# Optimization experiments

Measured on AMD Instinct MI355X. Metric: run time of the kernel, lower is better.

The kernel has to match this reference:

```python
import jax, jax.numpy as jnp
import numpy as np

NEG_INF = -1e9

def apply_rope(x, positions, head_dim, theta):
    # x: [B, S, H, Dh]; positions: [S] int32
    half = head_dim // 2
    fraction = (2.0 / head_dim) * jnp.arange(half, dtype=jnp.float32)  # [Dh/2]
    timescale = theta ** fraction
    angle = positions.astype(jnp.float32)[:, None] / timescale  # [S, Dh/2]
    sin = jnp.sin(angle)[None, :, None, :]  # [1,S,1,Dh/2]
    cos = jnp.cos(angle)[None, :, None, :]
    x1, x2 = jnp.split(x, 2, axis=-1)
    out = jnp.concatenate([x1 * cos - x2 * sin, x2 * cos + x1 * sin], axis=-1)
    return out.astype(x.dtype)

def setup_inputs() -> dict:
    key = jax.random.key(0)
    B, S, D = 2, 2048, 2048
    Q, N, H = 16, 4, 128
    ks = jax.random.split(key, 5)
    scale = 1.0 / np.sqrt(D)
    return {
        "x": jax.random.normal(ks[0], (B, S, D), dtype=jnp.float32),
        "positions": jnp.arange(S, dtype=jnp.int32),
        "Wq": jax.random.normal(ks[1], (Q, D, H), dtype=jnp.float32) * scale,
        "Wk": jax.random.normal(ks[2], (N, D, H), dtype=jnp.float32) * scale,
        "Wv": jax.random.normal(ks[3], (N, D, H), dtype=jnp.float32) * scale,
        "Wo": jax.random.normal(ks[4], (Q, H, D), dtype=jnp.float32) * scale,
    }

def reference(x, positions, Wq, Wk, Wv, Wo):
    head_dim = Wq.shape[-1]
    theta = 10000.0
    head_repeats = Wq.shape[0] // Wk.shape[0]  # GQA repeat factor

    q_BSQH = jnp.einsum('BSD,QDH->BSQH', x, Wq)
    q_BSQH = apply_rope(q_BSQH, positions, head_dim, theta)
    k_BTNH = jnp.einsum('BSD,NDH->BSNH', x, Wk)
    k_BTNH = apply_rope(k_BTNH, positions, head_dim, theta)
    v_BTNH = jnp.einsum('BSD,NDH->BSNH', x, Wv)

    k_BTQH = jnp.repeat(k_BTNH, head_repeats, axis=2)
    v_BTQH = jnp.repeat(v_BTNH, head_repeats, axis=2)

    scores_BQST = jnp.einsum('BSQH,BTQH->BQST', q_BSQH, k_BTQH) / jnp.sqrt(
        jnp.asarray(head_dim, dtype=x.dtype))
    S = q_BSQH.shape[1]
    causal = jnp.tril(jnp.ones((1, 1, S, S), dtype=jnp.bool_))
    scores_BQST = jnp.where(causal, scores_BQST, NEG_INF)
    weights_BQST = jax.nn.softmax(scores_BQST, axis=-1)
    out_BSQH = jnp.einsum('BQST,BTQH->BSQH', weights_BQST, v_BTQH)
    o_BSD = jnp.einsum('BSQH,QHD->BSD', out_BSQH, Wo)
    return o_BSD
```

## Files before the change

### kernel.cpp

```cpp
#include <hip/hip_runtime.h>
#include <math.h>

#define BB 2
#define SS 2048
#define DD 2048
#define QH 16
#define NKV 4
#define HD 128
#define REP 4
#define NEG_INF_F (-1e9f)

typedef __bf16 bfrag __attribute__((ext_vector_type(8)));
typedef float  ffrag __attribute__((ext_vector_type(4)));

__device__ inline unsigned short f2bf(float f) {
    unsigned u = __builtin_bit_cast(unsigned, f);
    u += 0x7fff + ((u >> 16) & 1);
    return (unsigned short)(u >> 16);
}
__device__ inline float bf2f(unsigned short u) {
    unsigned v = (unsigned)u << 16;
    return __builtin_bit_cast(float, v);
}
__device__ inline bfrag ld_frag(const unsigned short* p) {
    uint4 u = *(const uint4*)p;
    return __builtin_bit_cast(bfrag, u);
}
__device__ inline void async16(const void* g, void* l) {
    __builtin_amdgcn_global_load_lds(
        (const __attribute__((address_space(1))) unsigned int*)g,
        (__attribute__((address_space(3))) unsigned int*)l, 16, 0, 0);
}
__device__ inline unsigned pkbf(float a, float b) {
    unsigned short ua = __builtin_bit_cast(unsigned short, (__bf16)a);
    unsigned short ub = __builtin_bit_cast(unsigned short, (__bf16)b);
    return (unsigned)ua | ((unsigned)ub << 16);
}

__global__ __launch_bounds__(256) void prep_kernel(
    const float* __restrict__ x, unsigned short* __restrict__ xb,
    const float* __restrict__ Wq, const float* __restrict__ Wk,
    const float* __restrict__ Wv, const float* __restrict__ Wo,
    unsigned short* __restrict__ Wqkvt, unsigned short* __restrict__ Wot)
{
    __shared__ float tile[32][33];
    const int blk = blockIdx.x;
    const int tid = threadIdx.x;

    if (blk < 4096) {
        const int i = blk * 2048 + tid * 8;
        float4 a = *(const float4*)(x + i);
        float4 b = *(const float4*)(x + i + 4);
        unsigned short o[8];
        o[0] = f2bf(a.x); o[1] = f2bf(a.y); o[2] = f2bf(a.z); o[3] = f2bf(a.w);
        o[4] = f2bf(b.x); o[5] = f2bf(b.y); o[6] = f2bf(b.z); o[7] = f2bf(b.w);
        *(uint4*)(xb + i) = *(uint4*)o;
        return;
    }

    const float* in;
    unsigned short* out;
    int R, C, bx, by;
    if (blk < 10240) {
        const int lw = blk - 4096;
        const int z  = lw >> 8;
        const int r  = lw & 255;
        bx = r & 3; by = r >> 2;
        R = 2048; C = 128;
        if (z < 16)      { in = Wq + (size_t)z * 2048 * 128;
                           out = Wqkvt + (size_t)z * 128 * 2048; }
        else if (z < 20) { in = Wk + (size_t)(z - 16) * 2048 * 128;
                           out = Wqkvt + (size_t)(16 + (z - 16)) * 128 * 2048; }
        else             { in = Wv + (size_t)(z - 20) * 2048 * 128;
                           out = Wqkvt + (size_t)(20 + (z - 20)) * 128 * 2048; }
    } else {
        const int lw = blk - 10240;
        bx = lw & 63; by = lw >> 6;
        R = 2048; C = 2048;
        in = Wo; out = Wot;
    }
    const int c0 = bx * 32, r0 = by * 32;
    const int tx = tid & 31, ty = tid >> 5;
    #pragma unroll
    for (int k = 0; k < 4; ++k)
        tile[ty + 8 * k][tx] = in[(size_t)(r0 + ty + 8 * k) * C + c0 + tx];
    __syncthreads();
    #pragma unroll
    for (int k = 0; k < 4; ++k)
        out[(size_t)(c0 + ty + 8 * k) * R + r0 + tx] =
            f2bf(tile[tx][ty + 8 * k]);
}

__global__ __launch_bounds__(256) void gemm_bt_kernel(
    const unsigned short* __restrict__ A,
    const unsigned short* __restrict__ Bt,
    unsigned short* __restrict__ q_out, unsigned short* __restrict__ k_out,
    unsigned short* __restrict__ vt_out, float* __restrict__ f_out,
    int mode)
{
    const int m0 = blockIdx.x * 128;
    const int n0 = blockIdx.y * 128;
    const int tid  = threadIdx.x;
    const int w    = tid >> 6, lane = tid & 63;
    const int l16  = lane & 15, quad = lane >> 4;
    const int wm = (w >> 1) * 64, wn = (w & 1) * 64;
    const int sw8 = l16 & 7;

    __shared__ unsigned short As[2][128 * 64];
    __shared__ unsigned short Bs[2][128 * 64];

    ffrag acc[4][4];
    #pragma unroll
    for (int mi = 0; mi < 4; ++mi)
        #pragma unroll
        for (int ni = 0; ni < 4; ++ni)
            acc[mi][ni] = (ffrag){0.f, 0.f, 0.f, 0.f};

    auto stage = [&](int d, int k0) {
        #pragma unroll
        for (int j = 0; j < 4; ++j) {
            const int i   = j * 256 + tid;
            const int row = i >> 3;
            const int sl  = (i & 7) ^ (row & 7);
            async16(&A [(size_t)(m0 + row) * 2048 + k0 + sl * 8],
                    (char*)&As[d][0] + i * 16);
            async16(&Bt[(size_t)(n0 + row) * 2048 + k0 + sl * 8],
                    (char*)&Bs[d][0] + i * 16);
        }
    };

    stage(0, 0);
    __syncthreads();
    int cur = 0;
    for (int k0 = 0; k0 < 2048; k0 += 64) {
        if (k0 + 64 < 2048) stage(cur ^ 1, k0 + 64);

        #pragma unroll
        for (int c2 = 0; c2 < 2; ++c2) {
            bfrag af[4], bfr[4];
            #pragma unroll
            for (int mi = 0; mi < 4; ++mi)
                af[mi] = ld_frag(&As[cur][(wm + mi * 16 + l16) * 64
                                          + (((c2 * 4 + quad) ^ sw8) * 8)]);
            #pragma unroll
            for (int ni = 0; ni < 4; ++ni)
                bfr[ni] = ld_frag(&Bs[cur][(wn + ni * 16 + l16) * 64
                                           + (((c2 * 4 + quad) ^ sw8) * 8)]);
            #pragma unroll
            for (int mi = 0; mi < 4; ++mi)
                #pragma unroll
                for (int ni = 0; ni < 4; ++ni)
                    acc[mi][ni] = __builtin_amdgcn_mfma_f32_16x16x32_bf16(
                        af[mi], bfr[ni], acc[mi][ni], 0, 0, 0);
        }

        __syncthreads();
        cur ^= 1;
    }

    if (mode == 0) {
        #pragma unroll
        for (int mi = 0; mi < 4; ++mi)
            #pragma unroll
            for (int ni = 0; ni < 4; ++ni) {
                const int col = n0 + wn + ni * 16 + l16;
                #pragma unroll
                for (int r = 0; r < 4; ++r) {
                    const int row = m0 + wm + mi * 16 + quad * 4 + r;
                    f_out[(size_t)row * 2048 + col] = acc[mi][ni][r];
                }
            }
    } else if (n0 < 2560) {
        unsigned short* dst;
        int colbase, stride;
        if (n0 < 2048)      { dst = q_out; colbase = n0;        stride = 2048; }
        else                { dst = k_out; colbase = n0 - 2048; stride = 512;  }
        #pragma unroll
        for (int mi = 0; mi < 4; ++mi)
            #pragma unroll
            for (int ni = 0; ni < 4; ++ni) {
                const int col = colbase + wn + ni * 16 + l16;
                #pragma unroll
                for (int r = 0; r < 4; ++r) {
                    const int row = m0 + wm + mi * 16 + quad * 4 + r;
                    dst[(size_t)row * stride + col] = f2bf(acc[mi][ni][r]);
                }
            }
    } else {
        const int c3 = n0 - 2560;
        #pragma unroll
        for (int mi = 0; mi < 4; ++mi)
            #pragma unroll
            for (int ni = 0; ni < 4; ++ni) {
                const int col = c3 + wn + ni * 16 + l16;
                const int nh = col >> 7, h = col & 127;
                const int row0 = m0 + wm + mi * 16 + quad * 4;
                const int b = row0 >> 11, s = row0 & 2047;
                unsigned short pk[4];
                #pragma unroll
                for (int r = 0; r < 4; ++r) pk[r] = f2bf(acc[mi][ni][r]);
                *(uint2*)&vt_out[(((size_t)b * NKV + nh) * HD + h) * SS + s] =
                    *(uint2*)pk;
            }
    }
}

__global__ void rope_kernel(unsigned short* __restrict__ q,
                            unsigned short* __restrict__ k,
                            const int* __restrict__ positions)
{
    const int qpairs = BB * SS * QH * 64;
    const int kpairs = BB * SS * NKV * 64;
    int idx = blockIdx.x * blockDim.x + threadIdx.x;
    unsigned short* base;
    int nh;
    if (idx < qpairs) { base = q; nh = QH; }
    else {
        idx -= qpairs;
        if (idx >= kpairs) return;
        base = k; nh = NKV;
    }
    const int hh   = idx & 63;
    const int rest = idx >> 6;
    const int head = rest % nh;
    const int bs   = rest / nh;
    const int s    = bs % SS;

    unsigned short* p = base + ((size_t)bs * nh + head) * HD;
    const float pos = (float)positions[s];
    const float inv_ts = powf(10000.0f, -(float)hh * (1.0f / 64.0f));
    const float angle = pos * inv_ts;
    const float sn = sinf(angle), cs = cosf(angle);
    const float sc_ = (nh == QH) ? 0.08838834764831845f : 1.0f;
    const float x1 = bf2f(p[hh]), x2 = bf2f(p[hh + 64]);
    p[hh]      = f2bf((x1 * cs - x2 * sn) * sc_);
    p[hh + 64] = f2bf((x2 * cs + x1 * sn) * sc_);
}

__global__ __launch_bounds__(256, 2) void attn_kernel(
    const unsigned short* __restrict__ qb,
    const unsigned short* __restrict__ kb,
    const unsigned short* __restrict__ vt,
    unsigned short* __restrict__ o)
{
    int f = blockIdx.y * 16 + blockIdx.x;
    f = (f & 7) * 64 + (f >> 3);
    const int bh = f >> 4;
    const int bx = f & 15;

    const int b  = bh / QH, qh = bh % QH;
    const int n  = qh / REP;

    const int tid  = threadIdx.x;
    const int w    = tid >> 6;
    const int lane = tid & 63;
    const int l16  = lane & 15;
    const int quad = lane >> 4;
    const int sw   = l16 & 7;

    __shared__ unsigned short Ks[2][2][64][64];
    __shared__ unsigned short Vs[2][128][64];
    __shared__ unsigned short Ps[4][16][72];

    const unsigned short* kbase = kb + (size_t)b * (SS * NKV * HD) + n * HD;
    const unsigned short* vbase = vt + ((size_t)b * NKV + n) * HD * SS;

    for (int ph = 0; ph < 2; ++ph) {
        const int tile = ph == 0 ? (31 - bx) : bx;
        const int s0 = tile * 64;
        const int rbase = s0 + w * 16 + quad * 4;
        const int thr   = w * 16 + l16;

        bfrag qf[4];
        {
            const unsigned short* qp =
                qb + ((size_t)(b * SS + s0 + w * 16 + l16) * QH + qh) * HD
                   + quad * 8;
            #pragma unroll
            for (int c = 0; c < 4; ++c) qf[c] = ld_frag(qp + c * 32);
        }
        ffrag oacc[8];
        #pragma unroll
        for (int t = 0; t < 8; ++t) oacc[t] = (ffrag){0.f, 0.f, 0.f, 0.f};
        float mr = -1e30f, lr = 0.0f;

        #pragma unroll
        for (int j = 0; j < 4; ++j) {
            const int s = j * 256 + tid;
            {   const int cc = s >> 9, t = (s >> 3) & 63;
                const int sl = (s & 7) ^ (t & 7);
                async16(kbase + (size_t)t * (NKV * HD) + cc * 64 + sl * 8,
                        (char*)&Ks[0][0][0][0] + s * 16);
            }
            {   const int h = s >> 3, sl = (s & 7) ^ (h & 7);
                async16(vbase + (size_t)h * SS + sl * 8,
                        (char*)&Vs[0][0][0] + s * 16);
            }
        }
        __syncthreads();

        int p = 0;
        for (int t0 = 0; t0 <= s0; t0 += 64, p ^= 1) {
            if (t0 + 64 <= s0) {
                const int tn = t0 + 64;
                #pragma unroll
                for (int j = 0; j < 4; ++j) {
                    const int s = j * 256 + tid;
                    {   const int cc = s >> 9, t = (s >> 3) & 63;
                        const int sl = (s & 7) ^ (t & 7);
                        async16(kbase + (size_t)(tn + t) * (NKV * HD)
                                      + cc * 64 + sl * 8,
                                (char*)&Ks[p ^ 1][0][0][0] + s * 16);
                    }
                    {   const int h = s >> 3, sl = (s & 7) ^ (h & 7);
                        async16(vbase + (size_t)h * SS + tn + sl * 8,
                                (char*)&Vs[p ^ 1][0][0] + s * 16);
                    }
                }
            }

            ffrag sc[4];
            #pragma unroll
            for (int t = 0; t < 4; ++t) sc[t] = (ffrag){0.f, 0.f, 0.f, 0.f};
            __builtin_amdgcn_s_setprio(1);
            #pragma unroll
            for (int c = 0; c < 4; ++c) {
                const int cc = c >> 1, cb = (c & 1) * 4;
                #pragma unroll
                for (int t = 0; t < 4; ++t) {
                    bfrag kfr = ld_frag(
                        &Ks[p][cc][t * 16 + l16][((cb + quad) ^ sw) * 8]);
                    sc[t] = __builtin_amdgcn_mfma_f32_16x16x32_bf16(
                        kfr, qf[c], sc[t], 0, 0, 0);
                }
            }
            __builtin_amdgcn_s_setprio(0);

            const bool diag = (t0 == s0);
            if (diag) {
                #pragma unroll
                for (int t = 0; t < 4; ++t) {
                    const int col0 = t * 16 + quad * 4;
                    #pragma unroll
                    for (int r = 0; r < 4; ++r)
                        if (col0 + r > thr) sc[t][r] = NEG_INF_F;
                }
            }

            float tmax;
            {
                float a0 = fmaxf(fmaxf(sc[0][0], sc[0][1]),
                                 fmaxf(sc[0][2], sc[0][3]));
                float a1 = fmaxf(fmaxf(sc[1][0], sc[1][1]),
                                 fmaxf(sc[1][2], sc[1][3]));
                float a2 = fmaxf(fmaxf(sc[2][0], sc[2][1]),
                                 fmaxf(sc[2][2], sc[2][3]));
                float a3 = fmaxf(fmaxf(sc[3][0], sc[3][1]),
                                 fmaxf(sc[3][2], sc[3][3]));
                tmax = fmaxf(fmaxf(a0, a1), fmaxf(a2, a3));
            }
            tmax = fmaxf(tmax, __shfl_xor(tmax, 16));
            tmax = fmaxf(tmax, __shfl_xor(tmax, 32));

            if (__any(tmax > mr + 8.0f)) {
                const float mnew  = fmaxf(mr, tmax);
                const float alpha = __expf(mr - mnew);
                lr *= alpha;
                mr = mnew;
                #pragma unroll
                for (int r = 0; r < 4; ++r) {
                    const float ar =
                        __shfl(alpha, (lane & 48) | (quad * 4 + r));
                    #pragma unroll
                    for (int t = 0; t < 8; ++t) oacc[t][r] *= ar;
                }
            }

            float ps = 0.f;
            #pragma unroll
            for (int t = 0; t < 4; ++t) {
                const float p0 = __expf(sc[t][0] - mr);
                const float p1 = __expf(sc[t][1] - mr);
                const float p2 = __expf(sc[t][2] - mr);
                const float p3 = __expf(sc[t][3] - mr);
                ps += (p0 + p1) + (p2 + p3);
                uint2 pk2;
                pk2.x = pkbf(p0, p1);
                pk2.y = pkbf(p2, p3);
                *(uint2*)&Ps[w][l16][t * 16 + quad * 4] = pk2;
            }
            ps += __shfl_xor(ps, 16);
            ps += __shfl_xor(ps, 32);
            lr += ps;

            __builtin_amdgcn_s_setprio(1);
            #pragma unroll
            for (int c = 0; c < 2; ++c) {
                bfrag pf = ld_frag(&Ps[w][l16][c * 32 + quad * 8]);
                #pragma unroll
                for (int t = 0; t < 8; ++t) {
                    bfrag vf = ld_frag(
                        &Vs[p][t * 16 + l16][((c * 4 + quad) ^ sw) * 8]);
                    oacc[t] = __builtin_amdgcn_mfma_f32_16x16x32_bf16(
                        pf, vf, oacc[t], 0, 0, 0);
                }
            }
            __builtin_amdgcn_s_setprio(0);

            __syncthreads();
        }

        #pragma unroll
        for (int r = 0; r < 4; ++r) {
            const float lrr  = __shfl(lr, (lane & 48) | (quad * 4 + r));
            const float invl = 1.0f / lrr;
            const int row = rbase + r;
            unsigned short* op = o + ((size_t)(b * SS + row) * QH + qh) * HD;
            #pragma unroll
            for (int t = 0; t < 8; ++t)
                op[t * 16 + l16] = f2bf(oacc[t][r] * invl);
        }
    }
}

extern "C" void kernel_launch(void* const* d_in, const int* in_sizes, int n_in,
                              void* d_out, int out_size, void* d_ws,
                              size_t ws_size, hipStream_t stream)
{
    const float* x         = (const float*)d_in[0];
    const int*   positions = (const int*)d_in[1];
    const float* Wq        = (const float*)d_in[2];
    const float* Wk        = (const float*)d_in[3];
    const float* Wv        = (const float*)d_in[4];
    const float* Wo        = (const float*)d_in[5];
    float* out = (float*)d_out;

    char* ws = (char*)d_ws;
    unsigned short* xb    = (unsigned short*)ws;
    unsigned short* Wqkvt = (unsigned short*)(ws + (16u << 20));
    unsigned short* Wot   = (unsigned short*)(ws + (28u << 20));
    unsigned short* qbf   = (unsigned short*)(ws + (36u << 20));
    unsigned short* kbf   = (unsigned short*)(ws + (52u << 20));
    unsigned short* vtb   = (unsigned short*)(ws + (56u << 20));
    unsigned short* opre  = xb;

    prep_kernel<<<14336, 256, 0, stream>>>(x, xb, Wq, Wk, Wv, Wo, Wqkvt, Wot);

    gemm_bt_kernel<<<dim3(32, 24), 256, 0, stream>>>(
        xb, Wqkvt, qbf, kbf, vtb, nullptr, 1);

    const int pairs = BB * SS * (QH + NKV) * 64;
    rope_kernel<<<(pairs + 255) / 256, 256, 0, stream>>>(qbf, kbf, positions);

    dim3 g2(16, BB * QH);
    attn_kernel<<<g2, 256, 0, stream>>>(qbf, kbf, vtb, opre);

    gemm_bt_kernel<<<dim3(32, 16), 256, 0, stream>>>(
        opre, Wot, nullptr, nullptr, nullptr, out, 0);
}
```

Before: 312.5 us.

## Shrink K tile to 32 keys, decouple K/V buffering, raise occupancy to three blocks

Splits the key loop into 32-key steps with K double-buffered per 32 keys while V stays at 64-key granularity, loading the next V tile every other step. Waves whose query rows lie entirely above a diagonal 32-key tile skip the score, softmax and PV work for it, which cuts wasted causal-masked compute. Shared-memory buffers shrink and launch bounds rise to 3 blocks per CU for more occupancy. The cost is twice as many barriers per key range and smaller MFMA batches per step, with register pressure capped by the tighter launch bound.

```diff
diff --git a/kernel.cpp b/kernel.cpp
--- a/kernel.cpp
+++ b/kernel.cpp
@@ -237,7 +237,7 @@
     p[hh + 64] = f2bf((x2 * cs + x1 * sn) * sc_);
 }
 
-__global__ __launch_bounds__(256, 2) void attn_kernel(
+__global__ __launch_bounds__(256, 3) void attn_kernel(
     const unsigned short* __restrict__ qb,
     const unsigned short* __restrict__ kb,
     const unsigned short* __restrict__ vt,
@@ -258,9 +258,9 @@
     const int quad = lane >> 4;
     const int sw   = l16 & 7;
 
-    __shared__ unsigned short Ks[2][2][64][64];
+    __shared__ unsigned short Ks[2][2][32][64];
     __shared__ unsigned short Vs[2][128][64];
-    __shared__ unsigned short Ps[4][16][72];
+    __shared__ unsigned short Ps[4][16][36];
 
     const unsigned short* kbase = kb + (size_t)b * (SS * NKV * HD) + n * HD;
     const unsigned short* vbase = vt + ((size_t)b * NKV + n) * HD * SS;
@@ -285,127 +285,130 @@
         float mr = -1e30f, lr = 0.0f;
 
         #pragma unroll
+        for (int j = 0; j < 2; ++j) {
+            const int i = j * 256 + tid;
+            const int cc = i >> 8, t = (i >> 3) & 31, sl = i & 7;
+            async16(kbase + (size_t)t * (NKV * HD) + cc * 64
+                          + ((sl ^ (t & 7)) * 8),
+                    (char*)&Ks[0][0][0][0] + i * 16);
+        }
+        #pragma unroll
         for (int j = 0; j < 4; ++j) {
-            const int s = j * 256 + tid;
-            {   const int cc = s >> 9, t = (s >> 3) & 63;
-                const int sl = (s & 7) ^ (t & 7);
-                async16(kbase + (size_t)t * (NKV * HD) + cc * 64 + sl * 8,
-                        (char*)&Ks[0][0][0][0] + s * 16);
-            }
-            {   const int h = s >> 3, sl = (s & 7) ^ (h & 7);
-                async16(vbase + (size_t)h * SS + sl * 8,
-                        (char*)&Vs[0][0][0] + s * 16);
-            }
+            const int i = j * 256 + tid;
+            const int h = i >> 3, sl = i & 7;
+            async16(vbase + (size_t)h * SS + ((sl ^ (h & 7)) * 8),
+                    (char*)&Vs[0][0][0] + i * 16);
         }
         __syncthreads();
 
-        int p = 0;
-        for (int t0 = 0; t0 <= s0; t0 += 64, p ^= 1) {
-            if (t0 + 64 <= s0) {
-                const int tn = t0 + 64;
+        for (int t0 = 0; t0 <= s0 + 32; t0 += 32) {
+            const int pk = (t0 >> 5) & 1;
+            const int pv = (t0 >> 6) & 1;
+
+            if (t0 <= s0) {
+                #pragma unroll
+                for (int j = 0; j < 2; ++j) {
+                    const int i = j * 256 + tid;
+                    const int cc = i >> 8, t = (i >> 3) & 31, sl = i & 7;
+                    async16(kbase + (size_t)(t0 + 32 + t) * (NKV * HD)
+                                  + cc * 64 + ((sl ^ (t & 7)) * 8),
+                            (char*)&Ks[pk ^ 1][0][0][0] + i * 16);
+                }
+            }
+            if ((t0 & 32) == 0 && t0 + 64 <= s0 + 32) {
                 #pragma unroll
                 for (int j = 0; j < 4; ++j) {
-                    const int s = j * 256 + tid;
-                    {   const int cc = s >> 9, t = (s >> 3) & 63;
-                        const int sl = (s & 7) ^ (t & 7);
-                        async16(kbase + (size_t)(tn + t) * (NKV * HD)
-                                      + cc * 64 + sl * 8,
-                                (char*)&Ks[p ^ 1][0][0][0] + s * 16);
+                    const int i = j * 256 + tid;
+                    const int h = i >> 3, sl = i & 7;
+                    async16(vbase + (size_t)h * SS + t0 + 64
+                                  + ((sl ^ (h & 7)) * 8),
+                            (char*)&Vs[pv ^ 1][0][0] + i * 16);
+                }
+            }
+
+            const int toff = t0 - s0;
+            if (toff <= w * 16 + 15) {
+                ffrag sc[2];
+                sc[0] = (ffrag){0.f, 0.f, 0.f, 0.f};
+                sc[1] = (ffrag){0.f, 0.f, 0.f, 0.f};
+                __builtin_amdgcn_s_setprio(1);
+                #pragma unroll
+                for (int c = 0; c < 4; ++c) {
+                    const int cc = c >> 1, cb = (c & 1) * 4;
+                    #pragma unroll
+                    for (int ts = 0; ts < 2; ++ts) {
+                        bfrag kfr = ld_frag(
+                            &Ks[pk][cc][ts * 16 + l16][((cb + quad) ^ sw) * 8]);
+                        sc[ts] = __builtin_amdgcn_mfma_f32_16x16x32_bf16(
+                            kfr, qf[c], sc[ts], 0, 0, 0);
                     }
-                    {   const int h = s >> 3, sl = (s & 7) ^ (h & 7);
-                        async16(vbase + (size_t)h * SS + tn + sl * 8,
-                                (char*)&Vs[p ^ 1][0][0] + s * 16);
+                }
+                __builtin_amdgcn_s_setprio(0);
+
+                if (toff >= 0) {
+                    #pragma unroll
+                    for (int ts = 0; ts < 2; ++ts) {
+                        const int col0 = toff + ts * 16 + quad * 4;
+                        #pragma unroll
+                        for (int r = 0; r < 4; ++r)
+                            if (col0 + r > thr) sc[ts][r] = NEG_INF_F;
                     }
                 }
-            }
-
-            ffrag sc[4];
-            #pragma unroll
-            for (int t = 0; t < 4; ++t) sc[t] = (ffrag){0.f, 0.f, 0.f, 0.f};
-            __builtin_amdgcn_s_setprio(1);
-            #pragma unroll
-            for (int c = 0; c < 4; ++c) {
-                const int cc = c >> 1, cb = (c & 1) * 4;
-                #pragma unroll
-                for (int t = 0; t < 4; ++t) {
-                    bfrag kfr = ld_frag(
-                        &Ks[p][cc][t * 16 + l16][((cb + quad) ^ sw) * 8]);
-                    sc[t] = __builtin_amdgcn_mfma_f32_16x16x32_bf16(
-                        kfr, qf[c], sc[t], 0, 0, 0);
-                }
-            }
-            __builtin_amdgcn_s_setprio(0);
-
-            const bool diag = (t0 == s0);
-            if (diag) {
-                #pragma unroll
-                for (int t = 0; t < 4; ++t) {
-                    const int col0 = t * 16 + quad * 4;
+
+                float tmax;
+                {
+                    float a0 = fmaxf(fmaxf(sc[0][0], sc[0][1]),
+                                     fmaxf(sc[0][2], sc[0][3]));
+                    float a1 = fmaxf(fmaxf(sc[1][0], sc[1][1]),
+                                     fmaxf(sc[1][2], sc[1][3]));
+                    tmax = fmaxf(a0, a1);
+                }
+                tmax = fmaxf(tmax, __shfl_xor(tmax, 16));
+                tmax = fmaxf(tmax, __shfl_xor(tmax, 32));
+
+                if (__any(tmax > mr + 8.0f)) {
+                    const float mnew  = fmaxf(mr, tmax);
+                    const float alpha = __expf(mr - mnew);
+                    lr *= alpha;
+                    mr = mnew;
                     #pragma unroll
-                    for (int r = 0; r < 4; ++r)
-                        if (col0 + r > thr) sc[t][r] = NEG_INF_F;
-                }
-            }
-
-            float tmax;
-            {
-                float a0 = fmaxf(fmaxf(sc[0][0], sc[0][1]),
-                                 fmaxf(sc[0][2], sc[0][3]));
-                float a1 = fmaxf(fmaxf(sc[1][0], sc[1][1]),
-                                 fmaxf(sc[1][2], sc[1][3]));
-                float a2 = fmaxf(fmaxf(sc[2][0], sc[2][1]),
-                                 fmaxf(sc[2][2], sc[2][3]));
-                float a3 = fmaxf(fmaxf(sc[3][0], sc[3][1]),
-                                 fmaxf(sc[3][2], sc[3][3]));
-                tmax = fmaxf(fmaxf(a0, a1), fmaxf(a2, a3));
-            }
-            tmax = fmaxf(tmax, __shfl_xor(tmax, 16));
-            tmax = fmaxf(tmax, __shfl_xor(tmax, 32));
-
-            if (__any(tmax > mr + 8.0f)) {
-                const float mnew  = fmaxf(mr, tmax);
-                const float alpha = __expf(mr - mnew);
-                lr *= alpha;
-                mr = mnew;
-                #pragma unroll
-                for (int r = 0; r < 4; ++r) {
-                    const float ar =
-                        __shfl(alpha, (lane & 48) | (quad * 4 + r));
-                    #pragma unroll
-                    for (int t = 0; t < 8; ++t) oacc[t][r] *= ar;
-                }
-            }
-
-            float ps = 0.f;
-            #pragma unroll
-            for (int t = 0; t < 4; ++t) {
-                const float p0 = __expf(sc[t][0] - mr);
-                const float p1 = __expf(sc[t][1] - mr);
-                const float p2 = __expf(sc[t][2] - mr);
-                const float p3 = __expf(sc[t][3] - mr);
-                ps += (p0 + p1) + (p2 + p3);
-                uint2 pk2;
-                pk2.x = pkbf(p0, p1);
-                pk2.y = pkbf(p2, p3);
-                *(uint2*)&Ps[w][l16][t * 16 + quad * 4] = pk2;
-            }
-            ps += __shfl_xor(ps, 16);
-            ps += __shfl_xor(ps, 32);
-            lr += ps;
-
-            __builtin_amdgcn_s_setprio(1);
-            #pragma unroll
-            for (int c = 0; c < 2; ++c) {
-                bfrag pf = ld_frag(&Ps[w][l16][c * 32 + quad * 8]);
+                    for (int r = 0; r < 4; ++r) {
+                        const float ar =
+                            __shfl(alpha, (lane & 48) | (quad * 4 + r));
+                        #pragma unroll
+                        for (int t = 0; t < 8; ++t) oacc[t][r] *= ar;
+                    }
+                }
+
+                float ps = 0.f;
+                #pragma unroll
+                for (int ts = 0; ts < 2; ++ts) {
+                    const float p0 = __expf(sc[ts][0] - mr);
+                    const float p1 = __expf(sc[ts][1] - mr);
+                    const float p2 = __expf(sc[ts][2] - mr);
+                    const float p3 = __expf(sc[ts][3] - mr);
+                    ps += (p0 + p1) + (p2 + p3);
+                    uint2 pk2;
+                    pk2.x = pkbf(p0, p1);
+                    pk2.y = pkbf(p2, p3);
+                    *(uint2*)&Ps[w][l16][ts * 16 + quad * 4] = pk2;
+                }
+                ps += __shfl_xor(ps, 16);
+                ps += __shfl_xor(ps, 32);
+                lr += ps;
+
+                const int sb = (t0 & 32) >> 3;
+                __builtin_amdgcn_s_setprio(1);
+                bfrag pf = ld_frag(&Ps[w][l16][quad * 8]);
                 #pragma unroll
                 for (int t = 0; t < 8; ++t) {
                     bfrag vf = ld_frag(
-                        &Vs[p][t * 16 + l16][((c * 4 + quad) ^ sw) * 8]);
+                        &Vs[pv][t * 16 + l16][((sb + quad) ^ sw) * 8]);
                     oacc[t] = __builtin_amdgcn_mfma_f32_16x16x32_bf16(
                         pf, vf, oacc[t], 0, 0, 0);
                 }
-            }
-            __builtin_amdgcn_s_setprio(0);
+                __builtin_amdgcn_s_setprio(0);
+            }
 
             __syncthreads();
         }
```

Measured after the change: 339.5 us. 1.09x slower.
